# Optimization experiments

Hardware: AMD Instinct MI355X
Metric: run time of the kernel (lower is better)

Reference implementation:

```python
import jax, jax.numpy as jnp
import numpy as np

B, L = 256, 8192
ACF_PAD = L - 1          # acf_class[1]
POOL = 8                 # acf_class[2]
ACF_SIZE = ACF_PAD + 1   # == L, length kept after trim
POOLED = ACF_SIZE // POOL  # 1024, MLP input size
LIN = [512, 256]
OUT = 4                  # no_reg=False -> 4 outputs


def _linear_init(key, fan_out, fan_in):
    kw, kb = jax.random.split(key)
    bound = 1.0 / np.sqrt(fan_in)
    W = jax.random.uniform(kw, (fan_out, fan_in), jnp.float32, -bound, bound)
    b = jax.random.uniform(kb, (fan_out,), jnp.float32, -bound, bound)
    return W, b


def setup_inputs() -> dict:
    key = jax.random.key(0)
    kx, k1, k2, k3 = jax.random.split(key, 4)
    x = jax.random.normal(kx, (B, 1, L), jnp.float32)
    W1, b1 = _linear_init(k1, LIN[0], POOLED)
    W2, b2 = _linear_init(k2, LIN[1], LIN[0])
    W3, b3 = _linear_init(k3, OUT, LIN[1])
    return {"x": x, "W1": W1, "b1": b1, "W2": W2, "b2": b2, "W3": W3, "b3": b3}


def reference(x, W1, b1, W2, b2, W3, b3):
    # x: [B, 1, L]. Grouped conv1d with groups=B == per-sample autocorrelation.
    a = x[:, 0, :]                                             # [B, L]
    # full cross-correlation of a with itself: [B, 2L-1], lags -(L-1)..(L-1)
    corr = jax.vmap(lambda v: jnp.correlate(v, v, mode="full"))(a)
    # trim [:, acf_pad:] keeps non-negative lags 0..L-1 -> length ACF_SIZE
    r = corr[:, L - 1:]                                        # [B, L]
    # MaxPool1d(POOL), stride == POOL, floor division (L divisible here)
    pooled = r.reshape(B, POOLED, POOL).max(axis=-1)           # [B, POOLED]
    # normalize by per-sample max
    norm = pooled / jnp.max(pooled, axis=1, keepdims=True)
    # MLP: (Dropout is identity at inference) Linear -> LeakyReLU x2 -> Linear
    h = jax.nn.leaky_relu(norm @ W1.T + b1, negative_slope=0.01)
    h = jax.nn.leaky_relu(h @ W2.T + b2, negative_slope=0.01)
    return h @ W3.T + b3                                       # [B, 4]
```

## Files before the change

### kernel.cpp

```cpp
#include <hip/hip_runtime.h>

typedef __attribute__((ext_vector_type(8))) short bf16x8;
typedef __attribute__((ext_vector_type(16))) float f32x16;

#define LN 8192
#define SA_ROWB 4240
#define SB_OFF  33920
#define SMEM_BYTES 65536

__device__ __forceinline__ unsigned short f2bf(float f) {
    unsigned int u = __float_as_uint(f);
    u += 0x7fffu + ((u >> 16) & 1u);
    return (unsigned short)(u >> 16);
}
__device__ __forceinline__ float lrelu(float v) { return v > 0.f ? v : 0.01f * v; }
__device__ __forceinline__ float gldx(const float* p, int i) { return (i >= 0 && i < LN) ? p[i] : 0.f; }

__global__ __launch_bounds__(1024)
void acf_kernel(const float* __restrict__ x, float* __restrict__ ws)
{
    __shared__ __align__(16) unsigned char smem[SMEM_BYTES];
    __shared__ float red[16];

    const int tid  = threadIdx.x;
    const int row  = blockIdx.x;
    const int lane = tid & 63;
    const int wv   = tid >> 6;
    const float* xr = x + (size_t)row * LN;

    const int jj = lane & 31;
    const int gp = lane >> 5;
    const int dd = lane & 7;
    const int hh = (lane >> 3) & 3;
    const int aoff_lane = dd * SA_ROWB + 64 + 16 * gp - 16 * hh;

    const int q  = wv & 3;
    const int p  = wv >> 2;
    const int T1 = p;
    const int T2 = 7 - p;
    const int s1 = 512 - 64 * p;
    const int s2 = 64 + 64 * p;

    for (int s = tid; s < 1156; s += 1024) {
        const int e0 = s * 8;
        float4 fa, fb;
        if (e0 + 7 < LN) {
            fa = *(const float4*)(xr + e0);
            fb = *(const float4*)(xr + e0 + 4);
        } else {
            fa = make_float4(gldx(xr,e0),   gldx(xr,e0+1), gldx(xr,e0+2), gldx(xr,e0+3));
            fb = make_float4(gldx(xr,e0+4), gldx(xr,e0+5), gldx(xr,e0+6), gldx(xr,e0+7));
        }
        uint4 pk;
        pk.x = (unsigned)f2bf(fa.x) | ((unsigned)f2bf(fa.y) << 16);
        pk.y = (unsigned)f2bf(fa.z) | ((unsigned)f2bf(fa.w) << 16);
        pk.z = (unsigned)f2bf(fb.x) | ((unsigned)f2bf(fb.y) << 16);
        pk.w = (unsigned)f2bf(fb.z) | ((unsigned)f2bf(fb.w) << 16);
        const int ph = s ^ ((s >> 3) & 7);
        *(uint4*)(smem + SB_OFF + ph * 16) = pk;
    }

    f32x16 acc1 = {}, acc2 = {};

    for (int ch = 0; ch < 4; ++ch) {
        const int tc = ch << 11;
        __syncthreads();
        if (tid < 528) {
            const int base = tc + 4 * tid - 40;
            float4 fa, fb, fc;
            if (base >= 0 && base + 11 < LN) {
                fa = *(const float4*)(xr + base);
                fb = *(const float4*)(xr + base + 4);
                fc = *(const float4*)(xr + base + 8);
            } else {
                fa = make_float4(gldx(xr,base),   gldx(xr,base+1), gldx(xr,base+2),  gldx(xr,base+3));
                fb = make_float4(gldx(xr,base+4), gldx(xr,base+5), gldx(xr,base+6),  gldx(xr,base+7));
                fc = make_float4(gldx(xr,base+8), gldx(xr,base+9), gldx(xr,base+10), gldx(xr,base+11));
            }
            unsigned short us[12];
            us[0]=f2bf(fa.x); us[1]=f2bf(fa.y); us[2]=f2bf(fa.z);  us[3]=f2bf(fa.w);
            us[4]=f2bf(fb.x); us[5]=f2bf(fb.y); us[6]=f2bf(fb.z);  us[7]=f2bf(fb.w);
            us[8]=f2bf(fc.x); us[9]=f2bf(fc.y); us[10]=f2bf(fc.z); us[11]=f2bf(fc.w);
            #pragma unroll
            for (int d = 0; d < 8; ++d) {
                unsigned long long pk = (unsigned long long)us[8-d]
                                      | ((unsigned long long)us[9-d]  << 16)
                                      | ((unsigned long long)us[10-d] << 32)
                                      | ((unsigned long long)us[11-d] << 48);
                *(unsigned long long*)(smem + d * SA_ROWB + 8 * tid) = pk;
            }
        }
        __syncthreads();

        const int c0 = ch * 128;
        int dD = s2 - c0; dD = dD < 0 ? 0 : (dD > 128 ? 128 : dD);
        int sLo = c0 > s2 ? c0 : s2;
        int sHi = (c0 + 128) < s1 ? (c0 + 128) : s1;
        int sS = sHi - sLo; if (sS < 0) sS = 0;
        const int wd0 = c0 + q * (dD >> 2),  wd1 = c0 + (q + 1) * (dD >> 2);
        const int ws0 = sLo + q * (sS >> 2), ws1 = sLo + (q + 1) * (sS >> 2);

        {
            const unsigned char* ap = smem + aoff_lane + 32 * (wd0 - c0);
            int S1 = 128 * T1 + 2 * wd0 + 4 * jj + gp;
            int S2 = 128 * T2 + 2 * wd0 + 4 * jj + gp;
            for (int mq = wd0; mq < wd1; mq += 4) {
                bf16x8 A[4], B1[4], B2[4];
                #pragma unroll
                for (int u = 0; u < 4; ++u) {
                    A[u] = *(const bf16x8*)(ap + 32 * u);
                    const int sa = S1 + 2 * u, sb = S2 + 2 * u;
                    B1[u] = *(const bf16x8*)(smem + SB_OFF + ((sa ^ ((sa >> 3) & 7)) << 4));
                    B2[u] = *(const bf16x8*)(smem + SB_OFF + ((sb ^ ((sb >> 3) & 7)) << 4));
                }
                #pragma unroll
                for (int u = 0; u < 4; ++u) {
                    acc1 = __builtin_amdgcn_mfma_f32_32x32x16_bf16(A[u], B1[u], acc1, 0, 0, 0);
                    acc2 = __builtin_amdgcn_mfma_f32_32x32x16_bf16(A[u], B2[u], acc2, 0, 0, 0);
                }
                ap += 128; S1 += 8; S2 += 8;
            }
        }
        {
            const unsigned char* ap = smem + aoff_lane + 32 * (ws0 - c0);
            int S1 = 128 * T1 + 2 * ws0 + 4 * jj + gp;
            for (int mq = ws0; mq < ws1; mq += 4) {
                bf16x8 A[4], B1[4];
                #pragma unroll
                for (int u = 0; u < 4; ++u) {
                    A[u] = *(const bf16x8*)(ap + 32 * u);
                    const int sa = S1 + 2 * u;
                    B1[u] = *(const bf16x8*)(smem + SB_OFF + ((sa ^ ((sa >> 3) & 7)) << 4));
                }
                #pragma unroll
                for (int u = 0; u < 4; ++u)
                    acc1 = __builtin_amdgcn_mfma_f32_32x32x16_bf16(A[u], B1[u], acc1, 0, 0, 0);
                ap += 128; S1 += 8;
            }
        }
    }

    __syncthreads();

    auto pwrite = [&](int T, int s, const f32x16& acc, bool add) {
        unsigned char* bp = smem + (T * 2 + s) * 4096 + jj * 128;
        #pragma unroll
        for (int rq = 0; rq < 4; ++rq) {
            const int bi = (2 * rq + gp) ^ (jj & 7);
            float4 w = make_float4(acc[4*rq], acc[4*rq+1], acc[4*rq+2], acc[4*rq+3]);
            float4* pp = (float4*)(bp + bi * 16);
            if (add) { float4 o = *pp; w.x += o.x; w.y += o.y; w.z += o.z; w.w += o.w; }
            *pp = w;
        }
    };
    if (q < 2) { pwrite(T1, q, acc1, false); pwrite(T2, q, acc2, false); }
    __syncthreads();
    if (q >= 2) { pwrite(T1, q - 2, acc1, true); pwrite(T2, q - 2, acc2, true); }
    __syncthreads();

    {
        const int T  = tid >> 7;
        const int j2 = (tid >> 2) & 31;
        const int rq = tid & 3;
        const unsigned char* b0 = smem + (T * 2) * 4096 + j2 * 128;
        const int biA = (2 * rq)     ^ (j2 & 7);
        const int biB = (2 * rq + 1) ^ (j2 & 7);
        float4 s0a = *(const float4*)(b0 + biA * 16);
        float4 s0b = *(const float4*)(b0 + biB * 16);
        float4 s1a = *(const float4*)(b0 + 4096 + biA * 16);
        float4 s1b = *(const float4*)(b0 + 4096 + biB * 16);
        float v0 = s0a.x + s1a.x, v1 = s0a.y + s1a.y, v2 = s0a.z + s1a.z, v3 = s0a.w + s1a.w;
        float v4 = s0b.x + s1b.x, v5 = s0b.y + s1b.y, v6 = s0b.z + s1b.z, v7 = s0b.w + s1b.w;
        float m = fmaxf(fmaxf(fmaxf(v0, v1), fmaxf(v2, v3)), fmaxf(fmaxf(v4, v5), fmaxf(v6, v7)));

        float mx = m;
        for (int off = 32; off > 0; off >>= 1) mx = fmaxf(mx, __shfl_xor(mx, off));
        if (lane == 0) red[wv] = mx;
        __syncthreads();
        float pmax = red[0];
        #pragma unroll
        for (int k = 1; k < 16; ++k) pmax = fmaxf(pmax, red[k]);
        ws[(size_t)row * 1024 + tid] = m * (1.0f / pmax);
    }
}

__global__ __launch_bounds__(1024)
void mlp1_kernel(const float* __restrict__ ws, const float* __restrict__ W1,
                 const float* __restrict__ b1, float* __restrict__ h1g)
{
    __shared__ __align__(16) float arow[16 * 1024];
    const int tid  = threadIdx.x;
    const int lane = tid & 63;
    const int wv   = tid >> 6;
    const int bn   = blockIdx.x & 15;
    const int rb   = blockIdx.x >> 4;

    const float4* src = (const float4*)(ws + (size_t)rb * 16384);
    float4* a4 = (float4*)arow;
    for (int i = tid; i < 4096; i += 1024) a4[i] = src[i];
    __syncthreads();

    const int n0 = bn * 32 + wv * 2;
    float acc0[16], acc1[16];
    #pragma unroll
    for (int r = 0; r < 16; ++r) { acc0[r] = 0.f; acc1[r] = 0.f; }

    const float4* w0p = (const float4*)(W1 + (size_t)n0 * 1024);
    const float4* w1p = (const float4*)(W1 + (size_t)(n0 + 1) * 1024);
    #pragma unroll
    for (int qq = 0; qq < 4; ++qq) {
        const int kq = lane + 64 * qq;
        float4 w0 = w0p[kq], w1 = w1p[kq];
        #pragma unroll
        for (int r = 0; r < 16; ++r) {
            float4 av = a4[r * 256 + kq];
            acc0[r] += w0.x*av.x + w0.y*av.y + w0.z*av.z + w0.w*av.w;
            acc1[r] += w1.x*av.x + w1.y*av.y + w1.z*av.z + w1.w*av.w;
        }
    }
    #pragma unroll
    for (int off = 32; off > 0; off >>= 1) {
        #pragma unroll
        for (int r = 0; r < 16; ++r) {
            acc0[r] += __shfl_xor(acc0[r], off);
            acc1[r] += __shfl_xor(acc1[r], off);
        }
    }

    if (lane == 0) {
        const float bb0 = b1[n0], bb1 = b1[n0 + 1];
        #pragma unroll
        for (int r = 0; r < 16; ++r) {
            float2 hv = make_float2(lrelu(acc0[r] + bb0), lrelu(acc1[r] + bb1));
            *(float2*)(h1g + (size_t)(rb * 16 + r) * 512 + n0) = hv;
        }
    }
}

__global__ __launch_bounds__(1024)
void mlp23_kernel(const float* __restrict__ h1g,
                  const float* __restrict__ W2, const float* __restrict__ b2,
                  const float* __restrict__ W3, const float* __restrict__ b3,
                  float* __restrict__ out)
{
    __shared__ __align__(16) float h1s[512];
    __shared__ __align__(16) float h2[256];
    const int tid  = threadIdx.x;
    const int lane = tid & 63;
    const int wv   = tid >> 6;
    const int row  = blockIdx.x;

    if (tid < 128) ((float4*)h1s)[tid] = ((const float4*)(h1g + (size_t)row * 512))[tid];
    __syncthreads();

    {
        const float4* a4 = (const float4*)h1s;
        float4 av0 = a4[lane], av1 = a4[lane + 64];
        #pragma unroll
        for (int n0 = 0; n0 < 16; n0 += 8) {
            const int nb = wv * 16 + n0;
            float s[8];
            #pragma unroll
            for (int u = 0; u < 8; ++u) {
                const float4* wr = (const float4*)(W2 + (size_t)(nb + u) * 512);
                float4 w0 = wr[lane], w1 = wr[lane + 64];
                float t0 = w0.x*av0.x + w0.y*av0.y + w0.z*av0.z + w0.w*av0.w;
                float t1 = w1.x*av1.x + w1.y*av1.y + w1.z*av1.z + w1.w*av1.w;
                s[u] = t0 + t1;
            }
            #pragma unroll
            for (int off = 32; off > 0; off >>= 1) {
                #pragma unroll
                for (int u = 0; u < 8; ++u) s[u] += __shfl_xor(s[u], off);
            }
            if (lane == 0) {
                #pragma unroll
                for (int u = 0; u < 8; ++u) h2[nb + u] = lrelu(s[u] + b2[nb + u]);
            }
        }
    }
    __syncthreads();

    if (wv < 4) {
        const float4 w = ((const float4*)(W3 + wv * 256))[lane];
        const float4 a = ((const float4*)h2)[lane];
        float s = w.x*a.x + w.y*a.y + w.z*a.z + w.w*a.w;
        for (int off = 32; off > 0; off >>= 1) s += __shfl_xor(s, off);
        if (lane == 0) out[row * 4 + wv] = s + b3[wv];
    }
}

extern "C" void kernel_launch(void* const* d_in, const int* in_sizes, int n_in,
                              void* d_out, int out_size, void* d_ws, size_t ws_size,
                              hipStream_t stream)
{
    const float* x  = (const float*)d_in[0];
    const float* W1 = (const float*)d_in[1];
    const float* b1 = (const float*)d_in[2];
    const float* W2 = (const float*)d_in[3];
    const float* b2 = (const float*)d_in[4];
    const float* W3 = (const float*)d_in[5];
    const float* b3 = (const float*)d_in[6];
    float* outp = (float*)d_out;
    float* wsn  = (float*)d_ws;
    float* h1g  = wsn + 256 * 1024;

    hipLaunchKernelGGL(acf_kernel,   dim3(256), dim3(1024), 0, stream, x, wsn);
    hipLaunchKernelGGL(mlp1_kernel,  dim3(256), dim3(1024), 0, stream, wsn, W1, b1, h1g);
    hipLaunchKernelGGL(mlp23_kernel, dim3(256), dim3(1024), 0, stream, h1g, W2, b2, W3, b3, outp);
}
```

Measured before the change: 56.00 us.

## Fuse ACF and MLP into one per-row kernel with bf16 W1

Merges the autocorrelation, the first linear layer and the last two linear layers into a single per-row kernel. Normalized features and hidden activations now stay in shared memory instead of going through global workspace. A small pre-kernel converts W1 to bf16 each call so every block streams half the bytes. In exchange, each of the 256 blocks re-reads all of W1 with no batching across rows, and the bf16 weights lower precision.

```diff
diff --git a/kernel.cpp b/kernel.cpp
--- a/kernel.cpp
+++ b/kernel.cpp
@@ -16,8 +16,33 @@
 __device__ __forceinline__ float lrelu(float v) { return v > 0.f ? v : 0.01f * v; }
 __device__ __forceinline__ float gldx(const float* p, int i) { return (i >= 0 && i < LN) ? p[i] : 0.f; }
 
+__device__ __forceinline__ void dot8bf(uint4 q, const float* nl, float& acc) {
+    acc += __uint_as_float(q.x << 16)          * nl[0];
+    acc += __uint_as_float(q.x & 0xffff0000u)  * nl[1];
+    acc += __uint_as_float(q.y << 16)          * nl[2];
+    acc += __uint_as_float(q.y & 0xffff0000u)  * nl[3];
+    acc += __uint_as_float(q.z << 16)          * nl[4];
+    acc += __uint_as_float(q.z & 0xffff0000u)  * nl[5];
+    acc += __uint_as_float(q.w << 16)          * nl[6];
+    acc += __uint_as_float(q.w & 0xffff0000u)  * nl[7];
+}
+
+__global__ __launch_bounds__(512)
+void conv_kernel(const float* __restrict__ W1, unsigned short* __restrict__ W1bf)
+{
+    const int idx = blockIdx.x * 512 + threadIdx.x;
+    float4 v = ((const float4*)W1)[idx];
+    ushort4 o;
+    o.x = f2bf(v.x); o.y = f2bf(v.y); o.z = f2bf(v.z); o.w = f2bf(v.w);
+    ((ushort4*)W1bf)[idx] = o;
+}
+
 __global__ __launch_bounds__(1024)
-void acf_kernel(const float* __restrict__ x, float* __restrict__ ws)
+void fused_kernel(const float* __restrict__ x,
+                  const unsigned short* __restrict__ W1bf, const float* __restrict__ b1,
+                  const float* __restrict__ W2, const float* __restrict__ b2,
+                  const float* __restrict__ W3, const float* __restrict__ b3,
+                  float* __restrict__ out)
 {
     __shared__ __align__(16) unsigned char smem[SMEM_BYTES];
     __shared__ float red[16];
@@ -158,6 +183,9 @@
     if (q >= 2) { pwrite(T1, q - 2, acc1, true); pwrite(T2, q - 2, acc2, true); }
     __syncthreads();
 
+    float* nrm = (float*)smem;
+    float* h1  = (float*)(smem + 4096);
+    float* h2  = (float*)(smem + 6144);
     {
         const int T  = tid >> 7;
         const int j2 = (tid >> 2) & 31;
@@ -180,81 +208,57 @@
         float pmax = red[0];
         #pragma unroll
         for (int k = 1; k < 16; ++k) pmax = fmaxf(pmax, red[k]);
-        ws[(size_t)row * 1024 + tid] = m * (1.0f / pmax);
-    }
-}
-
-__global__ __launch_bounds__(1024)
-void mlp1_kernel(const float* __restrict__ ws, const float* __restrict__ W1,
-                 const float* __restrict__ b1, float* __restrict__ h1g)
-{
-    __shared__ __align__(16) float arow[16 * 1024];
-    const int tid  = threadIdx.x;
-    const int lane = tid & 63;
-    const int wv   = tid >> 6;
-    const int bn   = blockIdx.x & 15;
-    const int rb   = blockIdx.x >> 4;
-
-    const float4* src = (const float4*)(ws + (size_t)rb * 16384);
-    float4* a4 = (float4*)arow;
-    for (int i = tid; i < 4096; i += 1024) a4[i] = src[i];
-    __syncthreads();
-
-    const int n0 = bn * 32 + wv * 2;
-    float acc0[16], acc1[16];
-    #pragma unroll
-    for (int r = 0; r < 16; ++r) { acc0[r] = 0.f; acc1[r] = 0.f; }
-
-    const float4* w0p = (const float4*)(W1 + (size_t)n0 * 1024);
-    const float4* w1p = (const float4*)(W1 + (size_t)(n0 + 1) * 1024);
-    #pragma unroll
-    for (int qq = 0; qq < 4; ++qq) {
-        const int kq = lane + 64 * qq;
-        float4 w0 = w0p[kq], w1 = w1p[kq];
-        #pragma unroll
-        for (int r = 0; r < 16; ++r) {
-            float4 av = a4[r * 256 + kq];
-            acc0[r] += w0.x*av.x + w0.y*av.y + w0.z*av.z + w0.w*av.w;
-            acc1[r] += w1.x*av.x + w1.y*av.y + w1.z*av.z + w1.w*av.w;
-        }
-    }
-    #pragma unroll
-    for (int off = 32; off > 0; off >>= 1) {
-        #pragma unroll
-        for (int r = 0; r < 16; ++r) {
-            acc0[r] += __shfl_xor(acc0[r], off);
-            acc1[r] += __shfl_xor(acc1[r], off);
-        }
-    }
-
-    if (lane == 0) {
-        const float bb0 = b1[n0], bb1 = b1[n0 + 1];
-        #pragma unroll
-        for (int r = 0; r < 16; ++r) {
-            float2 hv = make_float2(lrelu(acc0[r] + bb0), lrelu(acc1[r] + bb1));
-            *(float2*)(h1g + (size_t)(rb * 16 + r) * 512 + n0) = hv;
-        }
-    }
-}
-
-__global__ __launch_bounds__(1024)
-void mlp23_kernel(const float* __restrict__ h1g,
-                  const float* __restrict__ W2, const float* __restrict__ b2,
-                  const float* __restrict__ W3, const float* __restrict__ b3,
-                  float* __restrict__ out)
-{
-    __shared__ __align__(16) float h1s[512];
-    __shared__ __align__(16) float h2[256];
-    const int tid  = threadIdx.x;
-    const int lane = tid & 63;
-    const int wv   = tid >> 6;
-    const int row  = blockIdx.x;
-
-    if (tid < 128) ((float4*)h1s)[tid] = ((const float4*)(h1g + (size_t)row * 512))[tid];
+        nrm[tid] = m * (1.0f / pmax);
+    }
     __syncthreads();
 
     {
-        const float4* a4 = (const float4*)h1s;
+        float nlo[8], nhi[8];
+        {
+            const float4* n4 = (const float4*)nrm;
+            float4 a0 = n4[2 * lane], a1 = n4[2 * lane + 1];
+            float4 b0 = n4[128 + 2 * lane], b1v = n4[128 + 2 * lane + 1];
+            nlo[0]=a0.x; nlo[1]=a0.y; nlo[2]=a0.z; nlo[3]=a0.w;
+            nlo[4]=a1.x; nlo[5]=a1.y; nlo[6]=a1.z; nlo[7]=a1.w;
+            nhi[0]=b0.x; nhi[1]=b0.y; nhi[2]=b0.z; nhi[3]=b0.w;
+            nhi[4]=b1v.x; nhi[5]=b1v.y; nhi[6]=b1v.z; nhi[7]=b1v.w;
+        }
+        for (int n0 = 0; n0 < 32; n0 += 4) {
+            const int nb = wv * 32 + n0;
+            float s0 = 0.f, s1 = 0.f, s2v = 0.f, s3 = 0.f;
+            {
+                const uint4* r0 = (const uint4*)(W1bf + (size_t)nb * 1024);
+                const uint4* r1 = (const uint4*)(W1bf + (size_t)(nb + 1) * 1024);
+                const uint4* r2 = (const uint4*)(W1bf + (size_t)(nb + 2) * 1024);
+                const uint4* r3 = (const uint4*)(W1bf + (size_t)(nb + 3) * 1024);
+                uint4 qa0 = r0[lane], qb0 = r0[64 + lane];
+                uint4 qa1 = r1[lane], qb1 = r1[64 + lane];
+                uint4 qa2 = r2[lane], qb2 = r2[64 + lane];
+                uint4 qa3 = r3[lane], qb3 = r3[64 + lane];
+                dot8bf(qa0, nlo, s0); dot8bf(qb0, nhi, s0);
+                dot8bf(qa1, nlo, s1); dot8bf(qb1, nhi, s1);
+                dot8bf(qa2, nlo, s2v); dot8bf(qb2, nhi, s2v);
+                dot8bf(qa3, nlo, s3); dot8bf(qb3, nhi, s3);
+            }
+            #pragma unroll
+            for (int off = 32; off > 0; off >>= 1) {
+                s0 += __shfl_xor(s0, off);
+                s1 += __shfl_xor(s1, off);
+                s2v += __shfl_xor(s2v, off);
+                s3 += __shfl_xor(s3, off);
+            }
+            if (lane == 0) {
+                h1[nb]     = lrelu(s0 + b1[nb]);
+                h1[nb + 1] = lrelu(s1 + b1[nb + 1]);
+                h1[nb + 2] = lrelu(s2v + b1[nb + 2]);
+                h1[nb + 3] = lrelu(s3 + b1[nb + 3]);
+            }
+        }
+    }
+    __syncthreads();
+
+    {
+        const float4* a4 = (const float4*)h1;
         float4 av0 = a4[lane], av1 = a4[lane + 64];
         #pragma unroll
         for (int n0 = 0; n0 < 16; n0 += 8) {
@@ -302,10 +306,9 @@
     const float* W3 = (const float*)d_in[5];
     const float* b3 = (const float*)d_in[6];
     float* outp = (float*)d_out;
-    float* wsn  = (float*)d_ws;
-    float* h1g  = wsn + 256 * 1024;
-
-    hipLaunchKernelGGL(acf_kernel,   dim3(256), dim3(1024), 0, stream, x, wsn);
-    hipLaunchKernelGGL(mlp1_kernel,  dim3(256), dim3(1024), 0, stream, wsn, W1, b1, h1g);
-    hipLaunchKernelGGL(mlp23_kernel, dim3(256), dim3(1024), 0, stream, h1g, W2, b2, W3, b3, outp);
-}
+    unsigned short* W1bf = (unsigned short*)d_ws;
+
+    hipLaunchKernelGGL(conv_kernel,  dim3(256), dim3(512),  0, stream, W1, W1bf);
+    hipLaunchKernelGGL(fused_kernel, dim3(256), dim3(1024), 0, stream,
+                       x, W1bf, b1, W2, b2, W3, b3, outp);
+}
```

Result: faster. 49.84 us (-11.0%).
